# Kernel optimization log

Hardware: AMD Instinct MI355X
Metric: run time of the kernel (lower is better)

Reference implementation:

```python
import math
import jax, jax.numpy as jnp
import numpy as np

N_HEADS = 16
D_EMBED = 1024
D_HEAD = D_EMBED // N_HEADS
BATCH = 2
SEQ = 2048


def setup_inputs() -> dict:
    key = jax.random.key(0)
    k1, k2, k3 = jax.random.split(key, 3)
    scale = 1.0 / math.sqrt(D_EMBED)
    return {
        "x": jax.random.normal(k1, (1, BATCH, SEQ, D_EMBED), dtype=jnp.float32),
        "w_in": jax.random.normal(k2, (3 * D_EMBED, D_EMBED), dtype=jnp.float32) * scale,
        "b_in": jnp.zeros((3 * D_EMBED,), dtype=jnp.float32),
        "w_out": jax.random.normal(k3, (D_EMBED, D_EMBED), dtype=jnp.float32) * scale,
        "b_out": jnp.zeros((D_EMBED,), dtype=jnp.float32),
        "causal_mask": 1,
    }


def reference(x, w_in, b_in, w_out, b_out, causal_mask):
    lead, B, S, D = x.shape  # lead == 1
    H, dh = N_HEADS, D_HEAD
    # fused QKV projection (torch Linear: x @ W^T + b)
    qkv = jnp.einsum("lbsd,ed->lbse", x, w_in) + b_in
    q, k, v = jnp.split(qkv, 3, axis=-1)
    # [1,B,S,D] -> [B,H,S,dh]
    def to_heads(t):
        return t.reshape(B, S, H, dh).transpose(0, 2, 1, 3)
    q, k, v = to_heads(q), to_heads(k), to_heads(v)
    # scaled dot-product attention with optional causal mask
    scores = jnp.einsum("bhqd,bhkd->bhqk", q, k)
    if causal_mask:
        mask = jnp.triu(jnp.ones((S, S), dtype=bool), k=1)
        scores = jnp.where(mask, -jnp.inf, scores)
    scores = scores / math.sqrt(dh)
    attn = jax.nn.softmax(scores, axis=-1)
    out = jnp.einsum("bhqk,bhkd->bhqd", attn, v)
    out = out.transpose(0, 2, 1, 3).reshape(lead, B, S, D)
    return jnp.einsum("lbsd,ed->lbse", out, w_out) + b_out
```

## Files before the change

kernel.cpp:

```cpp
#include <hip/hip_runtime.h>
#include <hip/hip_bf16.h>
#include <stdint.h>

#define S_LEN 2048
#define D_EMB 1024
#define NHEAD 16
#define DHEAD 64
#define NBATCH 2
#define MROWS 4096

typedef __attribute__((ext_vector_type(8))) short bf16x8;
typedef __attribute__((ext_vector_type(4))) float f32x4;
typedef unsigned short u16;
typedef unsigned int u32;

__device__ __forceinline__ u16 f2bf(float f) {
  union { float f; u32 u; } v; v.f = f;
  u32 r = v.u + 0x7fffu + ((v.u >> 16) & 1u);
  return (u16)(r >> 16);
}

__device__ __forceinline__ void gl_lds16(const void* g, void* l) {
  __builtin_amdgcn_global_load_lds(
      (const __attribute__((address_space(1))) u32*)g,
      (__attribute__((address_space(3))) u32*)l, 16, 0, 0);
}

__device__ __forceinline__ int swz(int o) { return o ^ (((o >> 7) & 7) << 4); }

#define MFMA16(a, b, c) __builtin_amdgcn_mfma_f32_16x16x32_bf16((a), (b), (c), 0, 0, 0)

__global__ void cast_f32_bf16(const float* __restrict__ in, u16* __restrict__ out, int n4) {
  int i = blockIdx.x * blockDim.x + threadIdx.x;
  if (i < n4) {
    float4 v = reinterpret_cast<const float4*>(in)[i];
    ushort4 o;
    o.x = f2bf(v.x); o.y = f2bf(v.y); o.z = f2bf(v.z); o.w = f2bf(v.w);
    reinterpret_cast<ushort4*>(out)[i] = o;
  }
}

__launch_bounds__(512, 2)
__global__ void gemm8p_qkv(const u16* __restrict__ A, const u16* __restrict__ Bm,
                           const float* __restrict__ bias,
                           u16* __restrict__ q_out, u16* __restrict__ k_out,
                           u16* __restrict__ vt_out) {
  __shared__ __align__(16) u16 As[2][2][8192];
  __shared__ __align__(16) u16 Bs[2][2][8192];
  const int K = 1024;
  const int t = threadIdx.x, w = t >> 6, lane = t & 63;
  const int lr = lane & 15, lg = lane >> 4;

  const int bid = (int)blockIdx.y * 12 + (int)blockIdx.x;
  const int sbid = (bid & 7) * 24 + (bid >> 3);
  const int bx = sbid % 12, by = sbid / 12;
  const int m0 = by * 256, n0 = bx * 256;
  const int wr = w >> 2, wc = w & 3;

  f32x4 acc[8][4] = {};

  const u16* Ab = A + (size_t)(m0 + w * 8 + (lane >> 3)) * K + ((lane & 7) ^ (lane >> 3)) * 8;
  const u16* Bb = Bm + (size_t)(n0 + w * 8 + (lane >> 3)) * K + ((lane & 7) ^ (lane >> 3)) * 8;
#define STG_A(TT, H, CC) \
  gl_lds16(Ab + (size_t)((H)*128 + (CC)*64) * K + (TT)*64, &As[(TT)&1][H][(CC)*4096 + w * 512])
#define STG_B(TT, H, CC) \
  gl_lds16(Bb + (size_t)((H)*128 + (CC)*64) * K + (TT)*64, &Bs[(TT)&1][H][(CC)*4096 + w * 512])

  const int xorv = (lane & 7) << 4;
  const int ofk0 = (lg * 16) ^ xorv, ofk1 = (64 + lg * 16) ^ xorv;

  STG_A(0, 0, 0); STG_A(0, 0, 1); STG_A(0, 1, 0); STG_A(0, 1, 1);
  STG_B(0, 0, 0); STG_B(0, 0, 1); STG_B(0, 1, 0); STG_B(0, 1, 1);
  asm volatile("s_waitcnt vmcnt(0)" ::: "memory");
  __builtin_amdgcn_s_barrier();

  bf16x8 aF[4][2];
  bf16x8 bF[2][2][2];

  for (int tt = 0; tt < 16; tt++) {
    const char* Ah = (const char*)&As[tt & 1][wr][0];
    const char* Bh = (const char*)&Bs[tt & 1][wc >> 1][0];
    const int brow0 = (wc & 1) * 64;
    const bool pf = (tt + 1) < 16;

#pragma unroll
    for (int i = 0; i < 4; i++) {
      const int r = i * 16 + lr;
      aF[i][0] = *(const bf16x8*)(Ah + r * 128 + ofk0);
      aF[i][1] = *(const bf16x8*)(Ah + r * 128 + ofk1);
    }
#pragma unroll
    for (int j = 0; j < 2; j++) {
      const int r = brow0 + j * 16 + lr;
      bF[0][j][0] = *(const bf16x8*)(Bh + r * 128 + ofk0);
      bF[0][j][1] = *(const bf16x8*)(Bh + r * 128 + ofk1);
    }
    if (pf) { STG_A(tt + 1, 0, 0); STG_A(tt + 1, 0, 1); STG_A(tt + 1, 1, 0); STG_A(tt + 1, 1, 1); }
    __builtin_amdgcn_s_barrier();
    asm volatile("s_waitcnt lgkmcnt(0)" ::: "memory");
    __builtin_amdgcn_sched_barrier(0);
    __builtin_amdgcn_s_setprio(1);
#pragma unroll
    for (int i = 0; i < 4; i++)
#pragma unroll
      for (int j = 0; j < 2; j++) {
        acc[i][j] = MFMA16(aF[i][0], bF[0][j][0], acc[i][j]);
        acc[i][j] = MFMA16(aF[i][1], bF[0][j][1], acc[i][j]);
      }
    __builtin_amdgcn_s_setprio(0);
    __builtin_amdgcn_s_barrier();

#pragma unroll
    for (int j = 0; j < 2; j++) {
      const int r = brow0 + (2 + j) * 16 + lr;
      bF[1][j][0] = *(const bf16x8*)(Bh + r * 128 + ofk0);
      bF[1][j][1] = *(const bf16x8*)(Bh + r * 128 + ofk1);
    }
    if (pf) { STG_B(tt + 1, 0, 0); STG_B(tt + 1, 0, 1); STG_B(tt + 1, 1, 0); STG_B(tt + 1, 1, 1); }
    __builtin_amdgcn_s_barrier();
    asm volatile("s_waitcnt lgkmcnt(0)" ::: "memory");
    __builtin_amdgcn_sched_barrier(0);
    __builtin_amdgcn_s_setprio(1);
#pragma unroll
    for (int i = 0; i < 4; i++)
#pragma unroll
      for (int j = 0; j < 2; j++) {
        acc[i][2 + j] = MFMA16(aF[i][0], bF[1][j][0], acc[i][2 + j]);
        acc[i][2 + j] = MFMA16(aF[i][1], bF[1][j][1], acc[i][2 + j]);
      }
    __builtin_amdgcn_s_setprio(0);
    __builtin_amdgcn_s_barrier();

#pragma unroll
    for (int i = 0; i < 4; i++) {
      const int r = 64 + i * 16 + lr;
      aF[i][0] = *(const bf16x8*)(Ah + r * 128 + ofk0);
      aF[i][1] = *(const bf16x8*)(Ah + r * 128 + ofk1);
    }
    __builtin_amdgcn_s_barrier();
    asm volatile("s_waitcnt lgkmcnt(0)" ::: "memory");
    __builtin_amdgcn_sched_barrier(0);
    __builtin_amdgcn_s_setprio(1);
#pragma unroll
    for (int i = 0; i < 4; i++)
#pragma unroll
      for (int j = 0; j < 2; j++) {
        acc[4 + i][2 + j] = MFMA16(aF[i][0], bF[1][j][0], acc[4 + i][2 + j]);
        acc[4 + i][2 + j] = MFMA16(aF[i][1], bF[1][j][1], acc[4 + i][2 + j]);
      }
    __builtin_amdgcn_s_setprio(0);
    __builtin_amdgcn_s_barrier();

    __builtin_amdgcn_s_setprio(1);
#pragma unroll
    for (int i = 0; i < 4; i++)
#pragma unroll
      for (int j = 0; j < 2; j++) {
        acc[4 + i][j] = MFMA16(aF[i][0], bF[0][j][0], acc[4 + i][j]);
        acc[4 + i][j] = MFMA16(aF[i][1], bF[0][j][1], acc[4 + i][j]);
      }
    __builtin_amdgcn_s_setprio(0);
    asm volatile("s_waitcnt vmcnt(0)" ::: "memory");
    __builtin_amdgcn_s_barrier();
  }
#undef STG_A
#undef STG_B

#pragma unroll
  for (int j = 0; j < 4; j++) {
    const int n = n0 + wc * 64 + j * 16 + lr;
    const float bv = bias[n];
    const int which = n >> 10, nn = n & 1023;
    const int h = nn >> 6, d = nn & 63;
#pragma unroll
    for (int i = 0; i < 8; i++) {
#pragma unroll
      for (int r = 0; r < 4; r++) {
        const int m = m0 + wr * 128 + i * 16 + lg * 4 + r;
        const int b = m >> 11, s = m & 2047;
        float v = acc[i][j][r] + bv;
        if (which == 0)
          q_out[(size_t)(((b * NHEAD + h) * S_LEN) + s) * DHEAD + d] = f2bf(v * 0.180336880f);
        else if (which == 1)
          k_out[(size_t)(((b * NHEAD + h) * S_LEN) + s) * DHEAD + d] = f2bf(v);
        else
          vt_out[(size_t)(((b * NHEAD + h) * DHEAD) + d) * S_LEN + s] = f2bf(v);
      }
    }
  }
}

__launch_bounds__(512, 2)
__global__ void gemm_pipe_f32(const u16* __restrict__ A, const u16* __restrict__ Bm,
                              const float* __restrict__ bias, int N,
                              float* __restrict__ f_out) {
  __shared__ __align__(16) u16 As[4][128 * 64];
  __shared__ __align__(16) u16 Bs[4][128 * 64];
  const int K = 1024, NT = 16;
  const int t = threadIdx.x, w = t >> 6, lane = t & 63;
  const int lr = lane & 15, lg = lane >> 4;
  const int m0 = blockIdx.y * 128, n0 = blockIdx.x * 128;
  const int wr = w >> 2, wc = w & 3;

  f32x4 acc[4][2] = {};

  const int srow = w * 8 + (lane >> 3);
  const int scol = ((lane & 7) ^ (lane >> 3)) * 8;
  const u16* Asrc = A + (size_t)(m0 + srow) * K + scol;
  const u16* Bsrc = Bm + (size_t)(n0 + srow) * K + scol;

#define STAGEP(T)                                                        \
  do {                                                                   \
    const int _kt = (T) * 64, _bf = (T) & 3;                             \
    gl_lds16(Asrc + _kt, &As[_bf][w * 512]);                             \
    gl_lds16(Asrc + (size_t)64 * K + _kt, &As[_bf][4096 + w * 512]);     \
    gl_lds16(Bsrc + _kt, &Bs[_bf][w * 512]);                             \
    gl_lds16(Bsrc + (size_t)64 * K + _kt, &Bs[_bf][4096 + w * 512]);     \
  } while (0)

  const int xorv = (lane & 7) << 4;
  const int ofk[2] = {(lg * 16) ^ xorv, (64 + lg * 16) ^ xorv};

  STAGEP(0);
  STAGEP(1);
  STAGEP(2);

  for (int kt = 0; kt < NT; kt++) {
    if (kt < NT - 2)       asm volatile("s_waitcnt vmcnt(8)" ::: "memory");
    else if (kt == NT - 2) asm volatile("s_waitcnt vmcnt(4)" ::: "memory");
    else                   asm volatile("s_waitcnt vmcnt(0)" ::: "memory");
    __builtin_amdgcn_s_barrier();

    if (kt + 3 < NT) STAGEP(kt + 3);

    const char* Ab = (const char*)&As[kt & 3][0];
    const char* Bb = (const char*)&Bs[kt & 3][0];
#pragma unroll
    for (int ks = 0; ks < 2; ks++) {
      bf16x8 bfr[2];
#pragma unroll
      for (int j = 0; j < 2; j++)
        bfr[j] = *(const bf16x8*)(Bb + (wc * 32 + j * 16 + lr) * 128 + ofk[ks]);
#pragma unroll
      for (int i = 0; i < 4; i++) {
        bf16x8 af = *(const bf16x8*)(Ab + (wr * 64 + i * 16 + lr) * 128 + ofk[ks]);
#pragma unroll
        for (int j = 0; j < 2; j++)
          acc[i][j] = MFMA16(af, bfr[j], acc[i][j]);
      }
    }
  }
#undef STAGEP

#pragma unroll
  for (int j = 0; j < 2; j++) {
    const int n = n0 + wc * 32 + j * 16 + lr;
    const float bv = bias[n];
#pragma unroll
    for (int i = 0; i < 4; i++) {
#pragma unroll
      for (int r = 0; r < 4; r++) {
        const int m = m0 + wr * 64 + i * 16 + lg * 4 + r;
        f_out[(size_t)m * N + n] = acc[i][j][r] + bv;
      }
    }
  }
}

__launch_bounds__(512, 2)
__global__ void attn_kernel(const u16* __restrict__ Qg, const u16* __restrict__ Kg,
                            const u16* __restrict__ Vtg, u16* __restrict__ AO,
                            const int* __restrict__ causal) {
  __shared__ __align__(16) u16 Kt[3][4096];
  __shared__ __align__(16) u16 Vt[3][4096];
  __shared__ __align__(16) u16 Pl[8][16 * 72];

  const int t = threadIdx.x, w = t >> 6, lane = t & 63;
  const int lr = lane & 15, lg = lane >> 4;
  const int nqt = (int)gridDim.x;
  const int qt = ((int)blockIdx.y < 16) ? (nqt - 1 - (int)blockIdx.x) : (int)blockIdx.x;
  const int bh = blockIdx.y;
  const size_t bh_off = (size_t)bh * S_LEN * DHEAD;
  const int cz = *causal;
  const int q0 = qt * 128;
  const int nk = cz ? (2 * qt + 2) : (S_LEN / 64);

  bf16x8 ones;
#pragma unroll
  for (int e = 0; e < 8; e++) ones[e] = (short)16256;

  {
    const char* qb = (const char*)(Qg + bh_off + (size_t)q0 * DHEAD);
#pragma unroll
    for (int c = 0; c < 2; c++) {
      int drel = c * 8192 + w * 1024 + lane * 16;
      gl_lds16(qb + swz(drel), (char*)&Kt[0][0] + c * 8192 + w * 1024);
    }
  }
  __syncthreads();
  bf16x8 qf[2];
#pragma unroll
  for (int ks = 0; ks < 2; ks++) {
    int rq = w * 16 + lr;
    qf[ks] = *(const bf16x8*)((const char*)&Kt[0][0] + swz(rq * 128 + ks * 64 + lg * 16));
  }
  __syncthreads();

  auto stageK = [&](int kt, int buf) {
    const char* kb = (const char*)(Kg + bh_off + (size_t)kt * 64 * DHEAD);
    int drel = w * 1024 + lane * 16;
    gl_lds16(kb + swz(drel), (char*)&Kt[buf][0] + w * 1024);
  };
  auto stageV = [&](int kt, int buf) {
    int drel = w * 1024 + lane * 16;
    int o = swz(drel);
    int row = o >> 7, colb = o & 127;
    const char* vb = (const char*)Vtg +
                     (((size_t)bh * DHEAD + row) * S_LEN + (size_t)kt * 64) * 2 + colb;
    gl_lds16(vb, (char*)&Vt[buf][0] + w * 1024);
  };

  float m_run[4], l_run[4];
  f32x4 o_acc[4] = {};
#pragma unroll
  for (int r = 0; r < 4; r++) { m_run[r] = -INFINITY; l_run[r] = 0.f; }

  stageK(0, 0); stageV(0, 0);
  stageK(1, 1); stageV(1, 1);

  int buf = 0;
  for (int kt = 0; kt < nk; kt++) {
    if (kt + 1 < nk) asm volatile("s_waitcnt vmcnt(2)" ::: "memory");
    else             asm volatile("s_waitcnt vmcnt(0)" ::: "memory");
    __builtin_amdgcn_s_barrier();
    __builtin_amdgcn_sched_barrier(0);

    if (kt + 2 < nk) {
      int b2 = buf + 2; if (b2 >= 3) b2 -= 3;
      stageK(kt + 2, b2);
      stageV(kt + 2, b2);
    }

    f32x4 s[4] = {};
#pragma unroll
    for (int nf = 0; nf < 4; nf++) {
#pragma unroll
      for (int ks = 0; ks < 2; ks++) {
        int r = nf * 16 + lr;
        bf16x8 kf = *(const bf16x8*)((const char*)&Kt[buf][0] + swz(r * 128 + ks * 64 + lg * 16));
        s[nf] = MFMA16(qf[ks], kf, s[nf]);
      }
    }

    if (cz && (kt * 64 + 63 > q0 + w * 16)) {
#pragma unroll
      for (int nf = 0; nf < 4; nf++)
#pragma unroll
        for (int r = 0; r < 4; r++) {
          int kv = kt * 64 + nf * 16 + lr;
          int qr = q0 + w * 16 + lg * 4 + r;
          if (kv > qr) s[nf][r] = -INFINITY;
        }
    }

    float lmax[4];
#pragma unroll
    for (int r = 0; r < 4; r++)
      lmax[r] = fmaxf(fmaxf(s[0][r], s[1][r]), fmaxf(s[2][r], s[3][r]));
    float need = fmaxf(fmaxf(lmax[0] - m_run[0], lmax[1] - m_run[1]),
                       fmaxf(lmax[2] - m_run[2], lmax[3] - m_run[3]));
    if (!__all(need <= 8.0f)) {
      float rmax[4];
#pragma unroll
      for (int r = 0; r < 4; r++) rmax[r] = lmax[r];
#pragma unroll
      for (int mlt = 1; mlt < 16; mlt <<= 1)
#pragma unroll
        for (int r = 0; r < 4; r++) rmax[r] = fmaxf(rmax[r], __shfl_xor(rmax[r], mlt, 64));
#pragma unroll
      for (int r = 0; r < 4; r++) {
        float mn = fmaxf(m_run[r], rmax[r]);
        float scl = exp2f(m_run[r] - mn);
        m_run[r] = mn;
        l_run[r] *= scl;
#pragma unroll
        for (int nf = 0; nf < 4; nf++) o_acc[nf][r] *= scl;
      }
    }

#pragma unroll
    for (int nf = 0; nf < 4; nf++)
#pragma unroll
      for (int r = 0; r < 4; r++) {
        float p = exp2f(s[nf][r] - m_run[r]);
        Pl[w][(lg * 4 + r) * 72 + nf * 16 + lr] = f2bf(p);
      }

    asm volatile("s_waitcnt lgkmcnt(0)" ::: "memory");
    __builtin_amdgcn_sched_barrier(0);

    bf16x8 pf[2];
#pragma unroll
    for (int ks = 0; ks < 2; ks++)
      pf[ks] = *(const bf16x8*)&Pl[w][lr * 72 + ks * 32 + lg * 8];

    f32x4 lsum = {};
    lsum = MFMA16(pf[0], ones, lsum);
    lsum = MFMA16(pf[1], ones, lsum);

#pragma unroll
    for (int nf = 0; nf < 4; nf++) {
#pragma unroll
      for (int ks = 0; ks < 2; ks++) {
        int r = nf * 16 + lr;
        bf16x8 vf = *(const bf16x8*)((const char*)&Vt[buf][0] + swz(r * 128 + ks * 64 + lg * 16));
        o_acc[nf] = MFMA16(pf[ks], vf, o_acc[nf]);
      }
    }
#pragma unroll
    for (int r = 0; r < 4; r++) l_run[r] += lsum[r];

    buf = (buf + 1 == 3) ? 0 : buf + 1;
  }

  const int b = bh >> 4, h = bh & 15;
#pragma unroll
  for (int nf = 0; nf < 4; nf++)
#pragma unroll
    for (int r = 0; r < 4; r++) {
      float v = o_acc[nf][r] / l_run[r];
      int qrow = q0 + w * 16 + lg * 4 + r;
      int d = nf * 16 + lr;
      AO[(size_t)(b * S_LEN + qrow) * D_EMB + h * DHEAD + d] = f2bf(v);
    }
}

extern "C" void kernel_launch(void* const* d_in, const int* in_sizes, int n_in,
                              void* d_out, int out_size, void* d_ws, size_t ws_size,
                              hipStream_t stream) {
  const float* x = (const float*)d_in[0];
  const float* w_in = (const float*)d_in[1];
  const float* b_in = (const float*)d_in[2];
  const float* w_out = (const float*)d_in[3];
  const float* b_out = (const float*)d_in[4];
  const int* causal = (const int*)d_in[5];
  float* out = (float*)d_out;

  char* p = (char*)d_ws;
  u16* xb = (u16*)p;  p += (size_t)MROWS * D_EMB * 2;
  u16* wib = (u16*)p; p += (size_t)3 * D_EMB * D_EMB * 2;
  u16* wob = (u16*)p; p += (size_t)D_EMB * D_EMB * 2;
  u16* Qg = (u16*)p;  p += (size_t)MROWS * D_EMB * 2;
  u16* Kg = (u16*)p;  p += (size_t)MROWS * D_EMB * 2;
  u16* Vtg = (u16*)p; p += (size_t)MROWS * D_EMB * 2;
  u16* AO = (u16*)p;  p += (size_t)MROWS * D_EMB * 2;

  {
    int n4 = MROWS * D_EMB / 4;
    cast_f32_bf16<<<(n4 + 255) / 256, 256, 0, stream>>>(x, xb, n4);
  }
  {
    int n4 = 3 * D_EMB * D_EMB / 4;
    cast_f32_bf16<<<(n4 + 255) / 256, 256, 0, stream>>>(w_in, wib, n4);
  }
  {
    int n4 = D_EMB * D_EMB / 4;
    cast_f32_bf16<<<(n4 + 255) / 256, 256, 0, stream>>>(w_out, wob, n4);
  }

  gemm8p_qkv<<<dim3(3 * D_EMB / 256, MROWS / 256), 512, 0, stream>>>(
      xb, wib, b_in, Qg, Kg, Vtg);

  attn_kernel<<<dim3(S_LEN / 128, NBATCH * NHEAD), 512, 0, stream>>>(Qg, Kg, Vtg, AO, causal);

  gemm_pipe_f32<<<dim3(D_EMB / 128, MROWS / 128), 512, 0, stream>>>(
      AO, wob, b_out, D_EMB, out);
}
```

Measured before the change: 223.3 us.

## Deepen QKV GEMM global-to-LDS prefetch to two tiles ahead

```diff
diff --git a/kernel.cpp b/kernel.cpp
--- a/kernel.cpp
+++ b/kernel.cpp
@@ -41,10 +41,10 @@
 }
 
 __launch_bounds__(512, 2)
-__global__ void gemm8p_qkv(const u16* __restrict__ A, const u16* __restrict__ Bm,
-                           const float* __restrict__ bias,
-                           u16* __restrict__ q_out, u16* __restrict__ k_out,
-                           u16* __restrict__ vt_out) {
+__global__ void gemm_ctr_qkv(const u16* __restrict__ A, const u16* __restrict__ Bm,
+                             const float* __restrict__ bias,
+                             u16* __restrict__ q_out, u16* __restrict__ k_out,
+                             u16* __restrict__ vt_out) {
   __shared__ __align__(16) u16 As[2][2][8192];
   __shared__ __align__(16) u16 Bs[2][2][8192];
   const int K = 1024;
@@ -61,17 +61,23 @@
 
   const u16* Ab = A + (size_t)(m0 + w * 8 + (lane >> 3)) * K + ((lane & 7) ^ (lane >> 3)) * 8;
   const u16* Bb = Bm + (size_t)(n0 + w * 8 + (lane >> 3)) * K + ((lane & 7) ^ (lane >> 3)) * 8;
-#define STG_A(TT, H, CC) \
-  gl_lds16(Ab + (size_t)((H)*128 + (CC)*64) * K + (TT)*64, &As[(TT)&1][H][(CC)*4096 + w * 512])
-#define STG_B(TT, H, CC) \
-  gl_lds16(Bb + (size_t)((H)*128 + (CC)*64) * K + (TT)*64, &Bs[(TT)&1][H][(CC)*4096 + w * 512])
+#define STG_A(TT, H)                                                                      \
+  do {                                                                                    \
+    gl_lds16(Ab + (size_t)((H) * 128) * K + (TT) * 64, &As[(TT)&1][H][w * 512]);          \
+    gl_lds16(Ab + (size_t)((H) * 128 + 64) * K + (TT) * 64, &As[(TT)&1][H][4096 + w * 512]); \
+  } while (0)
+#define STG_B(TT, H)                                                                      \
+  do {                                                                                    \
+    gl_lds16(Bb + (size_t)((H) * 128) * K + (TT) * 64, &Bs[(TT)&1][H][w * 512]);          \
+    gl_lds16(Bb + (size_t)((H) * 128 + 64) * K + (TT) * 64, &Bs[(TT)&1][H][4096 + w * 512]); \
+  } while (0)
 
   const int xorv = (lane & 7) << 4;
   const int ofk0 = (lg * 16) ^ xorv, ofk1 = (64 + lg * 16) ^ xorv;
 
-  STG_A(0, 0, 0); STG_A(0, 0, 1); STG_A(0, 1, 0); STG_A(0, 1, 1);
-  STG_B(0, 0, 0); STG_B(0, 0, 1); STG_B(0, 1, 0); STG_B(0, 1, 1);
-  asm volatile("s_waitcnt vmcnt(0)" ::: "memory");
+  STG_A(0, 0); STG_A(0, 1); STG_B(0, 0); STG_B(0, 1);
+  STG_A(1, 0); STG_A(1, 1); STG_B(1, 0); STG_B(1, 1);
+  asm volatile("s_waitcnt vmcnt(8)" ::: "memory");
   __builtin_amdgcn_s_barrier();
 
   bf16x8 aF[4][2];
@@ -81,7 +87,7 @@
     const char* Ah = (const char*)&As[tt & 1][wr][0];
     const char* Bh = (const char*)&Bs[tt & 1][wc >> 1][0];
     const int brow0 = (wc & 1) * 64;
-    const bool pf = (tt + 1) < 16;
+    const bool pf = (tt + 2) < 16;
 
 #pragma unroll
     for (int i = 0; i < 4; i++) {
@@ -95,7 +101,6 @@
       bF[0][j][0] = *(const bf16x8*)(Bh + r * 128 + ofk0);
       bF[0][j][1] = *(const bf16x8*)(Bh + r * 128 + ofk1);
     }
-    if (pf) { STG_A(tt + 1, 0, 0); STG_A(tt + 1, 0, 1); STG_A(tt + 1, 1, 0); STG_A(tt + 1, 1, 1); }
     __builtin_amdgcn_s_barrier();
     asm volatile("s_waitcnt lgkmcnt(0)" ::: "memory");
     __builtin_amdgcn_sched_barrier(0);
@@ -116,7 +121,6 @@
       bF[1][j][0] = *(const bf16x8*)(Bh + r * 128 + ofk0);
       bF[1][j][1] = *(const bf16x8*)(Bh + r * 128 + ofk1);
     }
-    if (pf) { STG_B(tt + 1, 0, 0); STG_B(tt + 1, 0, 1); STG_B(tt + 1, 1, 0); STG_B(tt + 1, 1, 1); }
     __builtin_amdgcn_s_barrier();
     asm volatile("s_waitcnt lgkmcnt(0)" ::: "memory");
     __builtin_amdgcn_sched_barrier(0);
@@ -137,6 +141,7 @@
       aF[i][0] = *(const bf16x8*)(Ah + r * 128 + ofk0);
       aF[i][1] = *(const bf16x8*)(Ah + r * 128 + ofk1);
     }
+    if (pf) { STG_B(tt + 2, 0); STG_B(tt + 2, 1); }
     __builtin_amdgcn_s_barrier();
     asm volatile("s_waitcnt lgkmcnt(0)" ::: "memory");
     __builtin_amdgcn_sched_barrier(0);
@@ -151,6 +156,7 @@
     __builtin_amdgcn_s_setprio(0);
     __builtin_amdgcn_s_barrier();
 
+    if (pf) { STG_A(tt + 2, 0); STG_A(tt + 2, 1); }
     __builtin_amdgcn_s_setprio(1);
 #pragma unroll
     for (int i = 0; i < 4; i++)
@@ -160,7 +166,10 @@
         acc[4 + i][j] = MFMA16(aF[i][1], bF[0][j][1], acc[4 + i][j]);
       }
     __builtin_amdgcn_s_setprio(0);
-    asm volatile("s_waitcnt vmcnt(0)" ::: "memory");
+    if (tt + 1 < 16) {
+      if (tt + 2 < 16) asm volatile("s_waitcnt vmcnt(8)" ::: "memory");
+      else             asm volatile("s_waitcnt vmcnt(0)" ::: "memory");
+    }
     __builtin_amdgcn_s_barrier();
   }
 #undef STG_A
@@ -468,7 +477,7 @@
     cast_f32_bf16<<<(n4 + 255) / 256, 256, 0, stream>>>(w_out, wob, n4);
   }
 
-  gemm8p_qkv<<<dim3(3 * D_EMB / 256, MROWS / 256), 512, 0, stream>>>(
+  gemm_ctr_qkv<<<dim3(3 * D_EMB / 256, MROWS / 256), 512, 0, stream>>>(
       xb, wib, b_in, Qg, Kg, Vtg);
 
   attn_kernel<<<dim3(S_LEN / 128, NBATCH * NHEAD), 512, 0, stream>>>(Qg, Kg, Vtg, AO, causal);
```

After: 228.6 us. 1.02x slower.
